# Kernel optimization log

Hardware: AMD Instinct MI355X
Metric: run time of the kernel (lower is better)

## Reference

```python
import jax, jax.numpy as jnp
import numpy as np

H = 1024      # hidden_size
V = 50257     # output_size (vocab)
L = 64        # max_length


def setup_inputs() -> dict:
    key = jax.random.key(0)
    ks = jax.random.split(key, 14)
    s = 1.0 / np.sqrt(H)
    return {
        "input": jax.random.randint(ks[0], (1,), 0, V, dtype=jnp.int64),
        "hidden": jax.random.normal(ks[1], (1, 1, H), dtype=jnp.float32),
        "encoder_outputs": jax.random.normal(ks[2], (L, H), dtype=jnp.float32),
        "emb": jax.random.normal(ks[3], (V, H), dtype=jnp.float32),
        "attn_W": jax.random.normal(ks[4], (L, 2 * H), dtype=jnp.float32) * s,
        "attn_b": jax.random.normal(ks[5], (L,), dtype=jnp.float32) * s,
        "comb_W": jax.random.normal(ks[6], (H, 2 * H), dtype=jnp.float32) * s,
        "comb_b": jax.random.normal(ks[7], (H,), dtype=jnp.float32) * s,
        "w_ih": jax.random.normal(ks[8], (3 * H, H), dtype=jnp.float32) * s,
        "w_hh": jax.random.normal(ks[9], (3 * H, H), dtype=jnp.float32) * s,
        "b_ih": jax.random.normal(ks[10], (3 * H,), dtype=jnp.float32) * s,
        "b_hh": jax.random.normal(ks[11], (3 * H,), dtype=jnp.float32) * s,
        "out_W": jax.random.normal(ks[12], (V, H), dtype=jnp.float32) * s,
        "out_b": jax.random.normal(ks[13], (V,), dtype=jnp.float32) * s,
    }


def reference(input, hidden, encoder_outputs, emb, attn_W, attn_b,
              comb_W, comb_b, w_ih, w_hh, b_ih, b_hh, out_W, out_b):
    # embedded: [1, H]  (dropout is identity, p effectively 0 at inference)
    embedded = emb[input[0]][None, :]
    h0 = hidden[0]  # [1, H]

    # additive-style attention over encoder_outputs [L, H]
    attn_logits = jnp.concatenate([embedded, h0], axis=1) @ attn_W.T + attn_b  # [1, L]
    attn_weights = jax.nn.softmax(attn_logits, axis=1)                          # [1, L]
    attn_applied = attn_weights @ encoder_outputs                               # [1, H]

    x = jnp.concatenate([embedded, attn_applied], axis=1) @ comb_W.T + comb_b  # [1, H]
    x = jax.nn.relu(x)

    # single-step GRU cell (PyTorch gate ordering: r, z, n)
    gi = x @ w_ih.T + b_ih    # [1, 3H]
    gh = h0 @ w_hh.T + b_hh   # [1, 3H]
    i_r, i_z, i_n = jnp.split(gi, 3, axis=1)
    h_r, h_z, h_n = jnp.split(gh, 3, axis=1)
    r = jax.nn.sigmoid(i_r + h_r)
    z = jax.nn.sigmoid(i_z + h_z)
    n = jnp.tanh(i_n + r * h_n)
    h_new = (1.0 - z) * n + z * h0  # [1, H]

    out = jax.nn.log_softmax(h_new @ out_W.T + out_b, axis=1)  # [1, V]
    return out, h_new[None, :, :], attn_weights
```

## Files before the change

kernel.cpp:

```cpp
#include <hip/hip_runtime.h>
#include <math.h>

constexpr int H = 1024;
constexpr int V = 50257;
constexpr int L = 64;

constexpr int OFF_ALOG = 0;
constexpr int OFF_XCAT = 64;
constexpr int OFF_X    = 2112;
constexpr int OFF_G    = 3136;
constexpr int OFF_LOG  = 9280;
constexpr int NBLK6    = (V + 15) / 16;
constexpr int OFF_PAIR = OFF_LOG + V;
constexpr int OFF_MS   = OFF_PAIR + 2 * NBLK6;

__global__ void k1_attn_logits(const int* __restrict__ idx_p,
                               const float* __restrict__ hid,
                               const float* __restrict__ emb,
                               const float* __restrict__ attn_W,
                               const float* __restrict__ attn_b,
                               float* __restrict__ ws) {
    const int l = blockIdx.x;
    const int tid = threadIdx.x;
    const int idx = idx_p[0];
    const float* wrow = attn_W + (size_t)l * (2 * H);
    const float* erow = emb + (size_t)idx * H;
    float acc = 0.f;
    for (int k = tid; k < 2 * H; k += 256) {
        float c = (k < H) ? erow[k] : hid[k - H];
        acc += wrow[k] * c;
    }
    for (int off = 32; off > 0; off >>= 1) acc += __shfl_down(acc, off);
    __shared__ float sred[4];
    const int lane = tid & 63, wid = tid >> 6;
    if (lane == 0) sred[wid] = acc;
    __syncthreads();
    if (tid == 0)
        ws[OFF_ALOG + l] = sred[0] + sred[1] + sred[2] + sred[3] + attn_b[l];
}

__global__ void k2_attn_apply(const int* __restrict__ idx_p,
                              const float* __restrict__ emb,
                              const float* __restrict__ enc,
                              float* __restrict__ ws,
                              float* __restrict__ out) {
    __shared__ float slog[L];
    __shared__ float wls[L];
    const int tid = threadIdx.x;
    const int col = blockIdx.x * 256 + tid;
    if (tid < L) slog[tid] = ws[OFF_ALOG + tid];
    __syncthreads();
    if (tid < L) {
        float m = -INFINITY;
        for (int i = 0; i < L; ++i) m = fmaxf(m, slog[i]);
        float s = 0.f;
        for (int i = 0; i < L; ++i) s += expf(slog[i] - m);
        wls[tid] = expf(slog[tid] - m) / s;
    }
    __syncthreads();
    if (blockIdx.x == 0 && tid < L) out[V + H + tid] = wls[tid];
    float acc = 0.f;
    for (int l = 0; l < L; ++l) acc += wls[l] * enc[l * H + col];
    const int idx = idx_p[0];
    ws[OFF_XCAT + col] = emb[(size_t)idx * H + col];
    ws[OFF_XCAT + H + col] = acc;
}

__global__ void k3_comb(const float* __restrict__ comb_W,
                        const float* __restrict__ comb_b,
                        float* __restrict__ ws) {
    __shared__ float4 sx[512];
    const int tid = threadIdx.x;
    const float4* xc4 = reinterpret_cast<const float4*>(ws + OFF_XCAT);
    sx[tid] = xc4[tid];
    sx[tid + 256] = xc4[tid + 256];
    __syncthreads();
    const int lane = tid & 63, wid = tid >> 6;
    const int row = blockIdx.x * 4 + wid;
    const float4* w4 = reinterpret_cast<const float4*>(comb_W + (size_t)row * (2 * H));
    float acc = 0.f;
#pragma unroll
    for (int it = 0; it < 8; ++it) {
        float4 a = w4[lane + it * 64];
        float4 b = sx[lane + it * 64];
        acc += a.x * b.x + a.y * b.y + a.z * b.z + a.w * b.w;
    }
    for (int off = 32; off > 0; off >>= 1) acc += __shfl_down(acc, off);
    if (lane == 0) ws[OFF_X + row] = fmaxf(acc + comb_b[row], 0.f);
}

__global__ void k4_gru_gemv(const float* __restrict__ w_ih,
                            const float* __restrict__ w_hh,
                            const float* __restrict__ b_ih,
                            const float* __restrict__ b_hh,
                            const float* __restrict__ hid,
                            float* __restrict__ ws) {
    __shared__ float4 sv[256];
    const int tid = threadIdx.x;
    const int row0 = blockIdx.x * 4;
    const bool is_h = (row0 >= 3 * H);
    const float* vec = is_h ? hid : (ws + OFF_X);
    sv[tid] = reinterpret_cast<const float4*>(vec)[tid];
    __syncthreads();
    const int lane = tid & 63, wid = tid >> 6;
    const int row = row0 + wid;
    const int lrow = is_h ? row - 3 * H : row;
    const float* W = is_h ? w_hh : w_ih;
    const float* B = is_h ? b_hh : b_ih;
    const float4* w4 = reinterpret_cast<const float4*>(W + (size_t)lrow * H);
    float acc = 0.f;
#pragma unroll
    for (int it = 0; it < 4; ++it) {
        float4 a = w4[lane + it * 64];
        float4 b = sv[lane + it * 64];
        acc += a.x * b.x + a.y * b.y + a.z * b.z + a.w * b.w;
    }
    for (int off = 32; off > 0; off >>= 1) acc += __shfl_down(acc, off);
    if (lane == 0) ws[OFF_G + row] = acc + B[lrow];
}

__global__ void k5_gates(const float* __restrict__ hid,
                         const float* __restrict__ ws,
                         float* __restrict__ out) {
    const int t = blockIdx.x * 256 + threadIdx.x;
    const float* g = ws + OFF_G;
    const float ir = g[t], iz = g[H + t], in_ = g[2 * H + t];
    const float hr = g[3 * H + t], hz = g[4 * H + t], hn = g[5 * H + t];
    const float r = 1.f / (1.f + expf(-(ir + hr)));
    const float z = 1.f / (1.f + expf(-(iz + hz)));
    const float n = tanhf(in_ + r * hn);
    out[V + t] = (1.f - z) * n + z * hid[t];
}

__global__ __launch_bounds__(1024) void k6_outproj(
        const float* __restrict__ out_W,
        const float* __restrict__ out_b,
        const float* __restrict__ hnew,
        float* __restrict__ ws) {
    __shared__ float4 sh[256];
    __shared__ float srow[16];
    const int tid = threadIdx.x;
    if (tid < 256) sh[tid] = reinterpret_cast<const float4*>(hnew)[tid];
    __syncthreads();
    const int lane = tid & 63, wid = tid >> 6;
    const int row = blockIdx.x * 16 + wid;
    float logit = -INFINITY;
    if (row < V) {
        const float4* w4 = reinterpret_cast<const float4*>(out_W + (size_t)row * H);
        float acc = 0.f;
#pragma unroll
        for (int it = 0; it < 4; ++it) {
            float4 a = w4[lane + it * 64];
            float4 b = sh[lane + it * 64];
            acc += a.x * b.x + a.y * b.y + a.z * b.z + a.w * b.w;
        }
        for (int off = 32; off > 0; off >>= 1) acc += __shfl_down(acc, off);
        if (lane == 0) {
            logit = acc + out_b[row];
            ws[OFF_LOG + row] = logit;
        }
    }
    if (lane == 0) srow[wid] = logit;
    __syncthreads();
    if (tid == 0) {
        float m = -INFINITY;
        for (int i = 0; i < 16; ++i) m = fmaxf(m, srow[i]);
        float s = 0.f;
        for (int i = 0; i < 16; ++i)
            if (srow[i] > -INFINITY) s += expf(srow[i] - m);
        ws[OFF_PAIR + 2 * blockIdx.x] = m;
        ws[OFF_PAIR + 2 * blockIdx.x + 1] = s;
    }
}

__global__ void k7_lse_combine(float* __restrict__ ws) {
    const int tid = threadIdx.x;
    float m = -INFINITY, s = 0.f;
    for (int i = tid; i < NBLK6; i += 256) {
        const float mi = ws[OFF_PAIR + 2 * i];
        const float si = ws[OFF_PAIR + 2 * i + 1];
        const float M = fmaxf(m, mi);
        s = s * expf(m - M) + si * expf(mi - M);
        m = M;
    }
    for (int off = 32; off > 0; off >>= 1) {
        const float mo = __shfl_down(m, off);
        const float so = __shfl_down(s, off);
        const float M = fmaxf(m, mo);
        s = s * expf(m - M) + so * expf(mo - M);
        m = M;
    }
    __shared__ float sm[4], ss[4];
    const int lane = tid & 63, wid = tid >> 6;
    if (lane == 0) { sm[wid] = m; ss[wid] = s; }
    __syncthreads();
    if (tid == 0) {
        float M = sm[0], S = ss[0];
        for (int i = 1; i < 4; ++i) {
            const float Mn = fmaxf(M, sm[i]);
            S = S * expf(M - Mn) + ss[i] * expf(sm[i] - Mn);
            M = Mn;
        }
        ws[OFF_MS] = M;
        ws[OFF_MS + 1] = logf(S);
    }
}

__global__ void k8_logsoftmax(const float* __restrict__ ws,
                              float* __restrict__ out) {
    const int i = blockIdx.x * 256 + threadIdx.x;
    if (i < V) out[i] = ws[OFF_LOG + i] - ws[OFF_MS] - ws[OFF_MS + 1];
}

extern "C" void kernel_launch(void* const* d_in, const int* in_sizes, int n_in,
                              void* d_out, int out_size, void* d_ws, size_t ws_size,
                              hipStream_t stream) {
    const int*   idx    = (const int*)d_in[0];
    const float* hid    = (const float*)d_in[1];
    const float* enc    = (const float*)d_in[2];
    const float* emb    = (const float*)d_in[3];
    const float* attn_W = (const float*)d_in[4];
    const float* attn_b = (const float*)d_in[5];
    const float* comb_W = (const float*)d_in[6];
    const float* comb_b = (const float*)d_in[7];
    const float* w_ih   = (const float*)d_in[8];
    const float* w_hh   = (const float*)d_in[9];
    const float* b_ih   = (const float*)d_in[10];
    const float* b_hh   = (const float*)d_in[11];
    const float* out_W  = (const float*)d_in[12];
    const float* out_b  = (const float*)d_in[13];
    float* out = (float*)d_out;
    float* ws  = (float*)d_ws;

    k1_attn_logits<<<L, 256, 0, stream>>>(idx, hid, emb, attn_W, attn_b, ws);
    k2_attn_apply<<<H / 256, 256, 0, stream>>>(idx, emb, enc, ws, out);
    k3_comb<<<H / 4, 256, 0, stream>>>(comb_W, comb_b, ws);
    k4_gru_gemv<<<(6 * H) / 4, 256, 0, stream>>>(w_ih, w_hh, b_ih, b_hh, hid, ws);
    k5_gates<<<H / 256, 256, 0, stream>>>(hid, ws, out);
    k6_outproj<<<NBLK6, 1024, 0, stream>>>(out_W, out_b, out + V, ws);
    k7_lse_combine<<<1, 256, 0, stream>>>(ws);
    k8_logsoftmax<<<(V + 255) / 256, 256, 0, stream>>>(ws, out);
}
```

Measured before the change: 64.50 us.

## Fuse decoder step into five kernels, overlapping hidden GEMV with attention

```diff
diff --git a/kernel.cpp b/kernel.cpp
--- a/kernel.cpp
+++ b/kernel.cpp
@@ -6,48 +6,70 @@
 constexpr int L = 64;
 
 constexpr int OFF_ALOG = 0;
-constexpr int OFF_XCAT = 64;
-constexpr int OFF_X    = 2112;
-constexpr int OFF_G    = 3136;
-constexpr int OFF_LOG  = 9280;
-constexpr int NBLK6    = (V + 15) / 16;
+constexpr int OFF_GH   = 64;
+constexpr int OFF_X    = 64 + 3 * H;
+constexpr int OFF_LOG  = OFF_X + H;
+constexpr int NBLKD    = (V + 15) / 16;
 constexpr int OFF_PAIR = OFF_LOG + V;
-constexpr int OFF_MS   = OFF_PAIR + 2 * NBLK6;
-
-__global__ void k1_attn_logits(const int* __restrict__ idx_p,
-                               const float* __restrict__ hid,
-                               const float* __restrict__ emb,
-                               const float* __restrict__ attn_W,
-                               const float* __restrict__ attn_b,
-                               float* __restrict__ ws) {
-    const int l = blockIdx.x;
-    const int tid = threadIdx.x;
-    const int idx = idx_p[0];
-    const float* wrow = attn_W + (size_t)l * (2 * H);
-    const float* erow = emb + (size_t)idx * H;
-    float acc = 0.f;
-    for (int k = tid; k < 2 * H; k += 256) {
-        float c = (k < H) ? erow[k] : hid[k - H];
-        acc += wrow[k] * c;
-    }
+
+__device__ __forceinline__ float wave_reduce(float acc) {
     for (int off = 32; off > 0; off >>= 1) acc += __shfl_down(acc, off);
-    __shared__ float sred[4];
-    const int lane = tid & 63, wid = tid >> 6;
-    if (lane == 0) sred[wid] = acc;
-    __syncthreads();
-    if (tid == 0)
-        ws[OFF_ALOG + l] = sred[0] + sred[1] + sred[2] + sred[3] + attn_b[l];
-}
-
-__global__ void k2_attn_apply(const int* __restrict__ idx_p,
-                              const float* __restrict__ emb,
-                              const float* __restrict__ enc,
-                              float* __restrict__ ws,
-                              float* __restrict__ out) {
+    return acc;
+}
+
+__device__ __forceinline__ float dot4(float4 a, float4 b) {
+    return a.x * b.x + a.y * b.y + a.z * b.z + a.w * b.w;
+}
+
+__global__ __launch_bounds__(256) void kA(const int* __restrict__ idx_p,
+                                          const float* __restrict__ hid,
+                                          const float* __restrict__ emb,
+                                          const float* __restrict__ attn_W,
+                                          const float* __restrict__ attn_b,
+                                          const float* __restrict__ w_hh,
+                                          const float* __restrict__ b_hh,
+                                          float* __restrict__ ws) {
+    const int tid = threadIdx.x;
+    const int lane = tid & 63, wid = tid >> 6;
+    if (blockIdx.x < 64) {
+        const int l = blockIdx.x;
+        const int idx = idx_p[0];
+        const float4* w4 = reinterpret_cast<const float4*>(attn_W + (size_t)l * (2 * H));
+        const float4* e4 = reinterpret_cast<const float4*>(emb + (size_t)idx * H);
+        const float4* h4 = reinterpret_cast<const float4*>(hid);
+        float acc = dot4(w4[tid], e4[tid]) + dot4(w4[tid + 256], h4[tid]);
+        acc = wave_reduce(acc);
+        __shared__ float sred[4];
+        if (lane == 0) sred[wid] = acc;
+        __syncthreads();
+        if (tid == 0)
+            ws[OFF_ALOG + l] = sred[0] + sred[1] + sred[2] + sred[3] + attn_b[l];
+    } else {
+        __shared__ float4 sv[256];
+        sv[tid] = reinterpret_cast<const float4*>(hid)[tid];
+        __syncthreads();
+        const int row = (blockIdx.x - 64) * 4 + wid;
+        const float4* w4 = reinterpret_cast<const float4*>(w_hh + (size_t)row * H);
+        float acc = 0.f;
+#pragma unroll
+        for (int it = 0; it < 4; ++it)
+            acc += dot4(w4[lane + it * 64], sv[lane + it * 64]);
+        acc = wave_reduce(acc);
+        if (lane == 0) ws[OFF_GH + row] = acc + b_hh[row];
+    }
+}
+
+__global__ __launch_bounds__(256) void kB(const int* __restrict__ idx_p,
+                                          const float* __restrict__ emb,
+                                          const float* __restrict__ enc,
+                                          const float* __restrict__ comb_W,
+                                          const float* __restrict__ comb_b,
+                                          float* __restrict__ ws,
+                                          float* __restrict__ out) {
     __shared__ float slog[L];
     __shared__ float wls[L];
-    const int tid = threadIdx.x;
-    const int col = blockIdx.x * 256 + tid;
+    __shared__ float4 sx[512];
+    const int tid = threadIdx.x;
     if (tid < L) slog[tid] = ws[OFF_ALOG + tid];
     __syncthreads();
     if (tid < L) {
@@ -56,87 +78,73 @@
         float s = 0.f;
         for (int i = 0; i < L; ++i) s += expf(slog[i] - m);
         wls[tid] = expf(slog[tid] - m) / s;
-    }
-    __syncthreads();
-    if (blockIdx.x == 0 && tid < L) out[V + H + tid] = wls[tid];
-    float acc = 0.f;
-    for (int l = 0; l < L; ++l) acc += wls[l] * enc[l * H + col];
+        if (blockIdx.x == 0) out[V + H + tid] = wls[tid];
+    }
+    __syncthreads();
     const int idx = idx_p[0];
-    ws[OFF_XCAT + col] = emb[(size_t)idx * H + col];
-    ws[OFF_XCAT + H + col] = acc;
-}
-
-__global__ void k3_comb(const float* __restrict__ comb_W,
-                        const float* __restrict__ comb_b,
-                        float* __restrict__ ws) {
-    __shared__ float4 sx[512];
-    const int tid = threadIdx.x;
-    const float4* xc4 = reinterpret_cast<const float4*>(ws + OFF_XCAT);
-    sx[tid] = xc4[tid];
-    sx[tid + 256] = xc4[tid + 256];
+    sx[tid] = reinterpret_cast<const float4*>(emb + (size_t)idx * H)[tid];
+    {
+        const float4* e4 = reinterpret_cast<const float4*>(enc);
+        float4 acc4 = {0.f, 0.f, 0.f, 0.f};
+#pragma unroll 8
+        for (int l = 0; l < L; ++l) {
+            const float w = wls[l];
+            const float4 v = e4[l * 256 + tid];
+            acc4.x += w * v.x; acc4.y += w * v.y;
+            acc4.z += w * v.z; acc4.w += w * v.w;
+        }
+        sx[256 + tid] = acc4;
+    }
     __syncthreads();
     const int lane = tid & 63, wid = tid >> 6;
     const int row = blockIdx.x * 4 + wid;
     const float4* w4 = reinterpret_cast<const float4*>(comb_W + (size_t)row * (2 * H));
     float acc = 0.f;
 #pragma unroll
-    for (int it = 0; it < 8; ++it) {
-        float4 a = w4[lane + it * 64];
-        float4 b = sx[lane + it * 64];
-        acc += a.x * b.x + a.y * b.y + a.z * b.z + a.w * b.w;
-    }
-    for (int off = 32; off > 0; off >>= 1) acc += __shfl_down(acc, off);
+    for (int it = 0; it < 8; ++it)
+        acc += dot4(w4[lane + it * 64], sx[lane + it * 64]);
+    acc = wave_reduce(acc);
     if (lane == 0) ws[OFF_X + row] = fmaxf(acc + comb_b[row], 0.f);
 }
 
-__global__ void k4_gru_gemv(const float* __restrict__ w_ih,
-                            const float* __restrict__ w_hh,
-                            const float* __restrict__ b_ih,
-                            const float* __restrict__ b_hh,
-                            const float* __restrict__ hid,
-                            float* __restrict__ ws) {
-    __shared__ float4 sv[256];
-    const int tid = threadIdx.x;
-    const int row0 = blockIdx.x * 4;
-    const bool is_h = (row0 >= 3 * H);
-    const float* vec = is_h ? hid : (ws + OFF_X);
-    sv[tid] = reinterpret_cast<const float4*>(vec)[tid];
-    __syncthreads();
-    const int lane = tid & 63, wid = tid >> 6;
-    const int row = row0 + wid;
-    const int lrow = is_h ? row - 3 * H : row;
-    const float* W = is_h ? w_hh : w_ih;
-    const float* B = is_h ? b_hh : b_ih;
-    const float4* w4 = reinterpret_cast<const float4*>(W + (size_t)lrow * H);
+__global__ __launch_bounds__(768) void kC(const float* __restrict__ w_ih,
+                                          const float* __restrict__ b_ih,
+                                          const float* __restrict__ hid,
+                                          float* __restrict__ ws,
+                                          float* __restrict__ out) {
+    __shared__ float4 sx4[256];
+    __shared__ float gi_s[12];
+    const int tid = threadIdx.x;
+    if (tid < 256) sx4[tid] = reinterpret_cast<const float4*>(ws + OFF_X)[tid];
+    __syncthreads();
+    const int lane = tid & 63, wid = tid >> 6;
+    const int g = wid >> 2, i = wid & 3;
+    const int row = g * H + blockIdx.x * 4 + i;
+    const float4* w4 = reinterpret_cast<const float4*>(w_ih + (size_t)row * H);
     float acc = 0.f;
 #pragma unroll
-    for (int it = 0; it < 4; ++it) {
-        float4 a = w4[lane + it * 64];
-        float4 b = sv[lane + it * 64];
-        acc += a.x * b.x + a.y * b.y + a.z * b.z + a.w * b.w;
-    }
-    for (int off = 32; off > 0; off >>= 1) acc += __shfl_down(acc, off);
-    if (lane == 0) ws[OFF_G + row] = acc + B[lrow];
-}
-
-__global__ void k5_gates(const float* __restrict__ hid,
-                         const float* __restrict__ ws,
-                         float* __restrict__ out) {
-    const int t = blockIdx.x * 256 + threadIdx.x;
-    const float* g = ws + OFF_G;
-    const float ir = g[t], iz = g[H + t], in_ = g[2 * H + t];
-    const float hr = g[3 * H + t], hz = g[4 * H + t], hn = g[5 * H + t];
-    const float r = 1.f / (1.f + expf(-(ir + hr)));
-    const float z = 1.f / (1.f + expf(-(iz + hz)));
-    const float n = tanhf(in_ + r * hn);
-    out[V + t] = (1.f - z) * n + z * hid[t];
-}
-
-__global__ __launch_bounds__(1024) void k6_outproj(
-        const float* __restrict__ out_W,
-        const float* __restrict__ out_b,
-        const float* __restrict__ hnew,
-        float* __restrict__ ws) {
+    for (int it = 0; it < 4; ++it)
+        acc += dot4(w4[lane + it * 64], sx4[lane + it * 64]);
+    acc = wave_reduce(acc);
+    if (lane == 0) gi_s[wid] = acc + b_ih[row];
+    __syncthreads();
+    if (tid < 4) {
+        const int t = blockIdx.x * 4 + tid;
+        const float ir = gi_s[tid], iz = gi_s[4 + tid], in_ = gi_s[8 + tid];
+        const float hr = ws[OFF_GH + t];
+        const float hz = ws[OFF_GH + H + t];
+        const float hn = ws[OFF_GH + 2 * H + t];
+        const float r = 1.f / (1.f + expf(-(ir + hr)));
+        const float z = 1.f / (1.f + expf(-(iz + hz)));
+        const float n = tanhf(in_ + r * hn);
+        out[V + t] = (1.f - z) * n + z * hid[t];
+    }
+}
+
+__global__ __launch_bounds__(1024) void kD(const float* __restrict__ out_W,
+                                           const float* __restrict__ out_b,
+                                           const float* __restrict__ hnew,
+                                           float* __restrict__ ws) {
     __shared__ float4 sh[256];
     __shared__ float srow[16];
     const int tid = threadIdx.x;
@@ -149,12 +157,9 @@
         const float4* w4 = reinterpret_cast<const float4*>(out_W + (size_t)row * H);
         float acc = 0.f;
 #pragma unroll
-        for (int it = 0; it < 4; ++it) {
-            float4 a = w4[lane + it * 64];
-            float4 b = sh[lane + it * 64];
-            acc += a.x * b.x + a.y * b.y + a.z * b.z + a.w * b.w;
-        }
-        for (int off = 32; off > 0; off >>= 1) acc += __shfl_down(acc, off);
+        for (int it = 0; it < 4; ++it)
+            acc += dot4(w4[lane + it * 64], sh[lane + it * 64]);
+        acc = wave_reduce(acc);
         if (lane == 0) {
             logit = acc + out_b[row];
             ws[OFF_LOG + row] = logit;
@@ -173,10 +178,11 @@
     }
 }
 
-__global__ void k7_lse_combine(float* __restrict__ ws) {
+__global__ __launch_bounds__(256) void kE(const float* __restrict__ ws,
+                                          float* __restrict__ out) {
     const int tid = threadIdx.x;
     float m = -INFINITY, s = 0.f;
-    for (int i = tid; i < NBLK6; i += 256) {
+    for (int i = tid; i < NBLKD; i += 256) {
         const float mi = ws[OFF_PAIR + 2 * i];
         const float si = ws[OFF_PAIR + 2 * i + 1];
         const float M = fmaxf(m, mi);
@@ -191,6 +197,7 @@
         m = M;
     }
     __shared__ float sm[4], ss[4];
+    __shared__ float fin[2];
     const int lane = tid & 63, wid = tid >> 6;
     if (lane == 0) { sm[wid] = m; ss[wid] = s; }
     __syncthreads();
@@ -201,15 +208,12 @@
             S = S * expf(M - Mn) + ss[i] * expf(sm[i] - Mn);
             M = Mn;
         }
-        ws[OFF_MS] = M;
-        ws[OFF_MS + 1] = logf(S);
-    }
-}
-
-__global__ void k8_logsoftmax(const float* __restrict__ ws,
-                              float* __restrict__ out) {
-    const int i = blockIdx.x * 256 + threadIdx.x;
-    if (i < V) out[i] = ws[OFF_LOG + i] - ws[OFF_MS] - ws[OFF_MS + 1];
+        fin[0] = M;
+        fin[1] = logf(S);
+    }
+    __syncthreads();
+    const int i = blockIdx.x * 256 + tid;
+    if (i < V) out[i] = ws[OFF_LOG + i] - fin[0] - fin[1];
 }
 
 extern "C" void kernel_launch(void* const* d_in, const int* in_sizes, int n_in,
@@ -232,12 +236,9 @@
     float* out = (float*)d_out;
     float* ws  = (float*)d_ws;
 
-    k1_attn_logits<<<L, 256, 0, stream>>>(idx, hid, emb, attn_W, attn_b, ws);
-    k2_attn_apply<<<H / 256, 256, 0, stream>>>(idx, emb, enc, ws, out);
-    k3_comb<<<H / 4, 256, 0, stream>>>(comb_W, comb_b, ws);
-    k4_gru_gemv<<<(6 * H) / 4, 256, 0, stream>>>(w_ih, w_hh, b_ih, b_hh, hid, ws);
-    k5_gates<<<H / 256, 256, 0, stream>>>(hid, ws, out);
-    k6_outproj<<<NBLK6, 1024, 0, stream>>>(out_W, out_b, out + V, ws);
-    k7_lse_combine<<<1, 256, 0, stream>>>(ws);
-    k8_logsoftmax<<<(V + 255) / 256, 256, 0, stream>>>(ws, out);
-}
+    kA<<<64 + 768, 256, 0, stream>>>(idx, hid, emb, attn_W, attn_b, w_hh, b_hh, ws);
+    kB<<<256, 256, 0, stream>>>(idx, emb, enc, comb_W, comb_b, ws, out);
+    kC<<<256, 768, 0, stream>>>(w_ih, b_ih, hid, ws, out);
+    kD<<<NBLKD, 1024, 0, stream>>>(out_W, out_b, out + V, ws);
+    kE<<<(V + 255) / 256, 256, 0, stream>>>(ws, out);
+}
```

After: 62.65 us. -2.9%, faster.
